# Optimization experiments

Measured on AMD Instinct MI355X. Metric: run time of the kernel, lower is better.

Reference implementation:

```python
import jax, jax.numpy as jnp
import numpy as np

T, B, L = 8, 4096, 50          # tables/features, batch, bag length
V, D = 100000, 128             # vocab per table, embedding dim


def setup_inputs() -> dict:
    key = jax.random.key(0)
    k_idx, k_tab = jax.random.split(key)
    indices = jax.random.randint(k_idx, (T, B, L), 0, V, dtype=jnp.int64)
    tables = jax.random.normal(k_tab, (T, V, D), dtype=jnp.float32)
    return {"indices": indices, "tables": tables}


def reference(indices, tables):
    # Per-table EmbeddingBag (mode='sum'): gather rows then pool each bag.
    # indices: [T, B, L] int, tables: [T, V, D] float
    gathered = jax.vmap(lambda tab, idx: tab[idx])(tables, indices)  # [T, B, L, D]
    pooled = gathered.sum(axis=2)                                    # [T, B, D]
    # Concatenate per-feature pooled embeddings along dim 1 -> [B, T*D]
    out = jnp.transpose(pooled, (1, 0, 2)).reshape(B, T * D)
    return out
```

## Files before the change

kernel.cpp:

```cpp
#include <hip/hip_runtime.h>


#define T_ 8
#define B_ 4096
#define L_ 50
#define V_ 100000
#define D_ 128
#define CHUNK 10

__global__ __launch_bounds__(256) void EmbeddingBagCollection_56959856279962_kernel(
    const int* __restrict__ indices,
    const float* __restrict__ tables,
    float* __restrict__ out)
{
    const int group = threadIdx.x >> 5;
    const int lane  = threadIdx.x & 31;
    const int bag0  = blockIdx.x << 3;
    const int t     = bag0 >> 12;
    const int bag   = bag0 + group;
    const int b     = bag & (B_ - 1);

    const int* __restrict__ idxp = indices + bag * L_;
    const float* __restrict__ tbl = tables + (size_t)t * (V_ * D_);

    float4 acc = make_float4(0.f, 0.f, 0.f, 0.f);

    int cur[CHUNK], nxt[CHUNK];
#pragma unroll
    for (int j = 0; j < CHUNK; ++j) cur[j] = idxp[j];

#pragma unroll
    for (int l = 0; l < L_; l += CHUNK) {
        if (l + CHUNK < L_) {
#pragma unroll
            for (int j = 0; j < CHUNK; ++j) nxt[j] = idxp[l + CHUNK + j];
        }
#pragma unroll
        for (int j = 0; j < CHUNK; ++j) {
            const unsigned off = ((unsigned)cur[j] << 9) | ((unsigned)lane << 4);
            const float4 v = *(const float4*)((const char*)tbl + off);
            acc.x += v.x; acc.y += v.y; acc.z += v.z; acc.w += v.w;
        }
#pragma unroll
        for (int j = 0; j < CHUNK; ++j) cur[j] = nxt[j];
    }

    float* __restrict__ op = out + b * (T_ * D_) + t * D_;
    ((float4*)op)[lane] = acc;
}

extern "C" void kernel_launch(void* const* d_in, const int* in_sizes, int n_in,
                              void* d_out, int out_size, void* d_ws, size_t ws_size,
                              hipStream_t stream) {
    const int*   indices = (const int*)d_in[0];
    const float* tables  = (const float*)d_in[1];
    float*       out     = (float*)d_out;

    const int grid = (T_ * B_) / 8;
    EmbeddingBagCollection_56959856279962_kernel<<<grid, 256, 0, stream>>>(
        indices, tables, out);
}
```

Baseline: 538.0 us.

## Stage bag indices in LDS and use rolling 16-deep row prefetch

The block's 400 indices are loaded cooperatively into shared memory with vectorized int4 loads, replacing per-lane scalar index loads from global memory. The gather loop becomes a rolling software pipeline that keeps 16 row loads in flight, and the output is written with a nontemporal store. The aim is more memory-level parallelism on the random row gathers and less redundant index traffic. In exchange it adds a block barrier and more vector registers for the prefetch buffer, which could lower occupancy.

```diff
diff --git a/kernel.cpp b/kernel.cpp
--- a/kernel.cpp
+++ b/kernel.cpp
@@ -6,47 +6,56 @@
 #define L_ 50
 #define V_ 100000
 #define D_ 128
-#define CHUNK 10
+#define PF 16
+
+typedef float nfloat4 __attribute__((ext_vector_type(4)));
 
 __global__ __launch_bounds__(256) void EmbeddingBagCollection_56959856279962_kernel(
     const int* __restrict__ indices,
     const float* __restrict__ tables,
     float* __restrict__ out)
 {
-    const int group = threadIdx.x >> 5;
-    const int lane  = threadIdx.x & 31;
-    const int bag0  = blockIdx.x << 3;
+    __shared__ int sidx[8 * L_];
+
+    const int tid  = threadIdx.x;
+    const int bag0 = blockIdx.x << 3;
+
+    const int* __restrict__ ip = indices + bag0 * L_;
+    if (tid < 100) {
+        ((int4*)sidx)[tid] = ((const int4*)ip)[tid];
+    }
+    __syncthreads();
+
+    const int group = tid >> 5;
+    const int lane  = tid & 31;
     const int t     = bag0 >> 12;
-    const int bag   = bag0 + group;
-    const int b     = bag & (B_ - 1);
+    const int b     = (bag0 + group) & (B_ - 1);
 
-    const int* __restrict__ idxp = indices + bag * L_;
     const float* __restrict__ tbl = tables + (size_t)t * (V_ * D_);
+    const int*   __restrict__ gi  = sidx + group * L_;
+    const unsigned laneoff = (unsigned)lane << 4;
 
-    float4 acc = make_float4(0.f, 0.f, 0.f, 0.f);
-
-    int cur[CHUNK], nxt[CHUNK];
-#pragma unroll
-    for (int j = 0; j < CHUNK; ++j) cur[j] = idxp[j];
+    nfloat4 acc = (nfloat4)(0.f);
+    nfloat4 buf[PF];
 
 #pragma unroll
-    for (int l = 0; l < L_; l += CHUNK) {
-        if (l + CHUNK < L_) {
-#pragma unroll
-            for (int j = 0; j < CHUNK; ++j) nxt[j] = idxp[l + CHUNK + j];
-        }
-#pragma unroll
-        for (int j = 0; j < CHUNK; ++j) {
-            const unsigned off = ((unsigned)cur[j] << 9) | ((unsigned)lane << 4);
-            const float4 v = *(const float4*)((const char*)tbl + off);
-            acc.x += v.x; acc.y += v.y; acc.z += v.z; acc.w += v.w;
-        }
-#pragma unroll
-        for (int j = 0; j < CHUNK; ++j) cur[j] = nxt[j];
+    for (int l = 0; l < PF; ++l) {
+        const unsigned off = ((unsigned)gi[l] << 9) | laneoff;
+        buf[l] = *(const nfloat4*)((const char*)tbl + off);
     }
 
-    float* __restrict__ op = out + b * (T_ * D_) + t * D_;
-    ((float4*)op)[lane] = acc;
+#pragma unroll
+    for (int l = 0; l < L_; ++l) {
+        const nfloat4 v = buf[l % PF];
+        if (l + PF < L_) {
+            const unsigned off = ((unsigned)gi[l + PF] << 9) | laneoff;
+            buf[l % PF] = *(const nfloat4*)((const char*)tbl + off);
+        }
+        acc += v;
+    }
+
+    nfloat4* __restrict__ op = (nfloat4*)(out + b * (T_ * D_) + t * D_) + lane;
+    __builtin_nontemporal_store(acc, op);
 }
 
 extern "C" void kernel_launch(void* const* d_in, const int* in_sizes, int n_in,
```

Result: no change. 538.5 us (+0.1%).
